# Kernel optimization log

Hardware: AMD Instinct MI355X
Metric: run time of the kernel (lower is better)

## Reference

```python
import jax, jax.numpy as jnp
import numpy as np

B, S, D = 4, 2048, 1024
H = 16
HD = D // H

def setup_inputs() -> dict:
    key = jax.random.key(0)
    ks = jax.random.split(key, 6)
    scale = 0.02
    return {
        "x": jax.random.normal(ks[0], (B, S, D), dtype=jnp.float32),
        "W_q": jax.random.normal(ks[1], (D, D), dtype=jnp.float32) * scale,
        "W_k": jax.random.normal(ks[2], (D, D), dtype=jnp.float32) * scale,
        "W_v": jax.random.normal(ks[3], (D, D), dtype=jnp.float32) * scale,
        "W_o": jax.random.normal(ks[4], (D, D), dtype=jnp.float32) * scale,
        "b_o": jax.random.normal(ks[5], (D,), dtype=jnp.float32) * scale,
    }

def reference(x, W_q, W_k, W_v, W_o, b_o):
    b, s, d = x.shape
    # projections, split heads: [b, h, s, hd]
    q = (x @ W_q).reshape(b, s, H, HD).transpose(0, 2, 1, 3)
    k = (x @ W_k).reshape(b, s, H, HD).transpose(0, 2, 1, 3)
    v = (x @ W_v).reshape(b, s, H, HD).transpose(0, 2, 1, 3)
    scores = jnp.einsum('bhqd,bhkd->bhqk', q, k)
    causal = jnp.triu(jnp.ones((s, s), dtype=bool), k=1)
    scores = jnp.where(causal, -jnp.inf, scores)
    # module divides by sqrt(hd) after masking; -inf stays -inf
    attn = jax.nn.softmax(scores / jnp.sqrt(jnp.float32(HD)), axis=-1)
    ctx = jnp.einsum('bhqk,bhkd->bhqd', attn, v)
    ctx = ctx.transpose(0, 2, 1, 3).reshape(b, s, d)
    return ctx @ W_o + b_o
```

## Files before the change

### kernel.cpp

```cpp
#include <hip/hip_runtime.h>
#include <hip/hip_bf16.h>
#include <math.h>

typedef __attribute__((ext_vector_type(8))) short bf16x8;
typedef __attribute__((ext_vector_type(4))) float f32x4;
typedef unsigned short u16;
typedef __hip_bfloat16 HB;

#define B_ 4
#define S_ 2048
#define D_ 1024
#define H_ 16
#define HD_ 64

__device__ __forceinline__ u16 f2b(float f) {
  HB h = __float2bfloat16(f);
  return *reinterpret_cast<u16*>(&h);
}
__device__ __forceinline__ void store1(HB* p, float v) { *p = __float2bfloat16(v); }
__device__ __forceinline__ void store1(float* p, float v) { *p = v; }

__device__ __forceinline__ float fexp2(float x) {
#if __has_builtin(__builtin_amdgcn_exp2f)
  return __builtin_amdgcn_exp2f(x);
#else
  return exp2f(x);
#endif
}

__device__ __forceinline__ void glds16(const u16* g, u16* l) {
  __builtin_amdgcn_global_load_lds(
      (const __attribute__((address_space(1))) void*)g,
      (__attribute__((address_space(3))) void*)l, 16, 0, 0);
}

__global__ __launch_bounds__(256) void cast_x(const float* __restrict__ xin,
                                              u16* __restrict__ xout) {
  const long i0 = ((long)blockIdx.x * 256 + threadIdx.x) * 8;
  bf16x8 r;
#pragma unroll
  for (int j = 0; j < 8; ++j) r[j] = (short)f2b(xin[i0 + j]);
  *(bf16x8*)(xout + i0) = r;
}

__global__ __launch_bounds__(256) void transpose_w(
    const float* __restrict__ w0, const float* __restrict__ w1,
    const float* __restrict__ w2, const float* __restrict__ w3,
    u16* __restrict__ out) {
  __shared__ __align__(16) u16 T[64 * 72];
  const float* Ws[4] = {w0, w1, w2, w3};
  const float* W = Ws[blockIdx.z];
  u16* Wt = out + (long)blockIdx.z * (1 << 20);
  const int t = threadIdx.x;
  const int r = t >> 3;
  const int c8 = (t & 7) * 8;
#pragma unroll
  for (int it = 0; it < 2; ++it) {
    const int row = blockIdx.y * 64 + it * 32 + r;
    const float* src = W + (long)row * D_ + blockIdx.x * 64 + c8;
#pragma unroll
    for (int j = 0; j < 8; ++j) T[(c8 + j) * 72 + it * 32 + r] = f2b(src[j]);
  }
  __syncthreads();
#pragma unroll
  for (int it = 0; it < 2; ++it) {
    const int row = it * 32 + r;
    bf16x8 v = *(const bf16x8*)(&T[row * 72 + c8]);
    *(bf16x8*)(Wt + (long)(blockIdx.x * 64 + row) * D_ + blockIdx.y * 64 + c8) = v;
  }
}

template <typename OT>
__global__ __launch_bounds__(256) void gemm_bt128d(
    const u16* __restrict__ A, const u16* __restrict__ BTb, long bt_stride,
    OT* __restrict__ Cb, long c_stride, const float* __restrict__ bias,
    u16* __restrict__ vt, int scale_q, int M, int N, int K) {
  const int flat = ((int)blockIdx.z << 9) + ((int)blockIdx.y << 3) + blockIdx.x;
  const int cpx = ((int)gridDim.z << 9) >> 3;
  const int nf = (flat & 7) * cpx + (flat >> 3);
  const int bz = nf >> 9;
  const int rem = nf & 511;
  const int by = rem >> 3, bx = rem & 7;

  const u16* BT = BTb + (long)bz * bt_stride;
  OT* C = Cb + (long)bz * c_stride;

  __shared__ __align__(16) u16 As[2][128 * 64];
  __shared__ __align__(16) u16 Bs[2][128 * 64];

  const int tid = threadIdx.x;
  const int w = tid >> 6, lane = tid & 63;
  const int qr = lane & 15, quad = lane >> 4;
  const int wm = w >> 1, wn = w & 1;

  const long rowA0 = (long)by * 128;
  const long rowB0 = (long)bx * 128;

  const int sr8 = lane >> 3;
  const int sc8 = ((lane & 7) ^ sr8) * 8;

  f32x4 acc[4][4] = {};

#define STAGE(nb, k0)                                                      \
  {                                                                        \
    _Pragma("unroll") for (int t = 0; t < 4; ++t) {                        \
      const int r = w * 32 + t * 8;                                        \
      glds16(A + (rowA0 + r + sr8) * K + (k0) + sc8, &As[nb][r * 64]);     \
      glds16(BT + (rowB0 + r + sr8) * K + (k0) + sc8, &Bs[nb][r * 64]);    \
    }                                                                      \
  }

  STAGE(0, 0);
  __syncthreads();

  const int NT = K >> 6;
  for (int kt = 0; kt < NT; ++kt) {
    const int b = kt & 1;
    if (kt + 1 < NT) STAGE(b ^ 1, (kt + 1) << 6);

#pragma unroll
    for (int kk = 0; kk < 2; ++kk) {
      bf16x8 af[4], bf[4];
#pragma unroll
      for (int ms = 0; ms < 4; ++ms) {
        const int m = wm * 64 + ms * 16 + qr;
        af[ms] = *(const bf16x8*)(&As[b][m * 64 +
                                         (((kk * 4 + quad) ^ (m & 7)) * 8)]);
      }
#pragma unroll
      for (int ns = 0; ns < 4; ++ns) {
        const int n = wn * 64 + ns * 16 + qr;
        bf[ns] = *(const bf16x8*)(&Bs[b][n * 64 +
                                         (((kk * 4 + quad) ^ (n & 7)) * 8)]);
      }
#pragma unroll
      for (int ms = 0; ms < 4; ++ms)
#pragma unroll
        for (int ns = 0; ns < 4; ++ns)
          acc[ms][ns] = __builtin_amdgcn_mfma_f32_16x16x32_bf16(
              af[ms], bf[ns], acc[ms][ns], 0, 0, 0);
    }
    __syncthreads();
  }
#undef STAGE

  if (vt && bz == 2) {
#pragma unroll
    for (int ns = 0; ns < 4; ++ns) {
      const int col = (int)rowB0 + wn * 64 + ns * 16 + qr;
#pragma unroll
      for (int ms = 0; ms < 4; ++ms) {
        const long row = rowA0 + wm * 64 + ms * 16 + quad * 4;
        const long b = row >> 11, s = row & 2047;
        ushort4 pk;
        pk.x = f2b(acc[ms][ns][0]); pk.y = f2b(acc[ms][ns][1]);
        pk.z = f2b(acc[ms][ns][2]); pk.w = f2b(acc[ms][ns][3]);
        *(ushort4*)(vt + ((b * H_ + (col >> 6)) * HD_ + (col & 63)) * S_ + s) = pk;
      }
    }
    return;
  }

  const float qs = (scale_q && bz == 0) ? 0.18033688011112042f : 1.f;
#pragma unroll
  for (int ns = 0; ns < 4; ++ns) {
    const long col = rowB0 + wn * 64 + ns * 16 + qr;
    const float bv = bias ? bias[col] : 0.f;
#pragma unroll
    for (int ms = 0; ms < 4; ++ms) {
      const long row = rowA0 + wm * 64 + ms * 16 + quad * 4;
#pragma unroll
      for (int r = 0; r < 4; ++r)
        store1(&C[(row + r) * (long)N + col], acc[ms][ns][r] * qs + bv);
    }
  }
}

__global__ __launch_bounds__(256) void attn12(
    const u16* __restrict__ Q, const u16* __restrict__ Kg,
    const u16* __restrict__ Vt, u16* __restrict__ ctx) {
  __shared__ __align__(16) u16 KV[2][2][64 * 64];
  __shared__ __align__(16) u16 Pl[4][16 * 64];

  const int tid = threadIdx.x;
  const int w = tid >> 6, lane = tid & 63;
  const int qr = lane & 15, quad = lane >> 4;
  const int bh = blockIdx.x;
  const int b = bh >> 4, h = bh & 15;

  const long baseQK = ((long)b * S_) * D_ + h * HD_;
  const long baseVt = (long)bh * HD_ * S_;

  const int sr8 = lane >> 3;
  const int sc8 = ((lane & 7) ^ sr8) * 8;

  bf16x8 vones;
#pragma unroll
  for (int j = 0; j < 8; ++j) vones[j] = (short)0x3F80;

  const int tiles2[2] = {(int)blockIdx.y, 15 - (int)blockIdx.y};

#pragma unroll
  for (int ti = 0; ti < 2; ++ti) {
    const int q0 = tiles2[ti] * 128;
    const int qbase = q0 + w * 32;

    bf16x8 aq[2][2];
#pragma unroll
    for (int i = 0; i < 2; ++i) {
      const u16* qp_ = Q + baseQK + (long)(qbase + i * 16 + qr) * D_;
      aq[i][0] = *(const bf16x8*)(qp_ + quad * 8);
      aq[i][1] = *(const bf16x8*)(qp_ + 32 + quad * 8);
    }

    f32x4 li[2] = {};
    f32x4 o[2][4] = {};

    const int nkt = q0 / 64 + 2;

#pragma unroll
    for (int t = 0; t < 2; ++t) {
      const int r = t * 32 + w * 8 + sr8;
      glds16(Kg + baseQK + (long)r * D_ + sc8, &KV[0][0][(t * 32 + w * 8) * 64]);
      glds16(Vt + baseVt + (long)r * S_ + sc8, &KV[0][1][(t * 32 + w * 8) * 64]);
    }

    for (int kt = 0; kt < nkt; ++kt) {
      const int kbase = kt * 64;
      const int buf = kt & 1;

      __syncthreads();

      if (kt + 1 < nkt) {
        const int nb = kbase + 64;
#pragma unroll
        for (int t = 0; t < 2; ++t) {
          const int r = t * 32 + w * 8 + sr8;
          glds16(Kg + baseQK + (long)(nb + r) * D_ + sc8,
                 &KV[buf ^ 1][0][(t * 32 + w * 8) * 64]);
          glds16(Vt + baseVt + (long)r * S_ + nb + sc8,
                 &KV[buf ^ 1][1][(t * 32 + w * 8) * 64]);
        }
      }

      const u16* Ksb = KV[buf][0];
      const u16* Vsb = KV[buf][1];

      bf16x8 kf[4][2];
#pragma unroll
      for (int ns = 0; ns < 4; ++ns) {
        const int row = ns * 16 + qr;
        kf[ns][0] = *(const bf16x8*)(&Ksb[row * 64 + ((quad ^ (row & 7)) * 8)]);
        kf[ns][1] =
            *(const bf16x8*)(&Ksb[row * 64 + (((4 + quad) ^ (row & 7)) * 8)]);
      }

      f32x4 s[2][4] = {};
#pragma unroll
      for (int i = 0; i < 2; ++i)
#pragma unroll
        for (int ns = 0; ns < 4; ++ns) {
          s[i][ns] = __builtin_amdgcn_mfma_f32_16x16x32_bf16(
              kf[ns][0], aq[i][0], s[i][ns], 0, 0, 0);
          s[i][ns] = __builtin_amdgcn_mfma_f32_16x16x32_bf16(
              kf[ns][1], aq[i][1], s[i][ns], 0, 0, 0);
        }

#pragma unroll
      for (int i = 0; i < 2; ++i) {
        if (kbase + 64 > qbase + i * 16) {
          const int qrow = qbase + i * 16 + qr;
#pragma unroll
          for (int ns = 0; ns < 4; ++ns) {
            const int kc = kbase + ns * 16 + quad * 4;
#pragma unroll
            for (int r = 0; r < 4; ++r)
              if (kc + r > qrow) s[i][ns][r] = -1.0e30f;
          }
        }
      }

      bf16x8 vf[4][2];
#pragma unroll
      for (int ns = 0; ns < 4; ++ns) {
        const int row = ns * 16 + qr;
        vf[ns][0] = *(const bf16x8*)(&Vsb[row * 64 + ((quad ^ (row & 7)) * 8)]);
        vf[ns][1] =
            *(const bf16x8*)(&Vsb[row * 64 + (((4 + quad) ^ (row & 7)) * 8)]);
      }

#pragma unroll
      for (int i = 0; i < 2; ++i) {
#pragma unroll
        for (int ns = 0; ns < 4; ++ns) {
          ushort4 pk;
          pk.x = f2b(fexp2(s[i][ns][0]));
          pk.y = f2b(fexp2(s[i][ns][1]));
          pk.z = f2b(fexp2(s[i][ns][2]));
          pk.w = f2b(fexp2(s[i][ns][3]));
          *(ushort4*)(&Pl[w][qr * 64 +
                             (((2 * ns + (quad >> 1)) ^ (qr & 7)) * 8) +
                             (quad & 1) * 4]) = pk;
        }

        bf16x8 pf0 = *(const bf16x8*)(&Pl[w][qr * 64 + ((quad ^ (qr & 7)) * 8)]);
        bf16x8 pf1 =
            *(const bf16x8*)(&Pl[w][qr * 64 + (((4 + quad) ^ (qr & 7)) * 8)]);
#pragma unroll
        for (int ns = 0; ns < 4; ++ns) {
          o[i][ns] = __builtin_amdgcn_mfma_f32_16x16x32_bf16(pf0, vf[ns][0],
                                                             o[i][ns], 0, 0, 0);
          o[i][ns] = __builtin_amdgcn_mfma_f32_16x16x32_bf16(pf1, vf[ns][1],
                                                             o[i][ns], 0, 0, 0);
        }
        li[i] =
            __builtin_amdgcn_mfma_f32_16x16x32_bf16(pf0, vones, li[i], 0, 0, 0);
        li[i] =
            __builtin_amdgcn_mfma_f32_16x16x32_bf16(pf1, vones, li[i], 0, 0, 0);
      }
    }

#pragma unroll
    for (int i = 0; i < 2; ++i)
#pragma unroll
      for (int r = 0; r < 4; ++r) {
        const float inv = 1.f / li[i][r];
        const long row = qbase + i * 16 + quad * 4 + r;
#pragma unroll
        for (int ns = 0; ns < 4; ++ns)
          ctx[((long)b * S_ + row) * D_ + h * HD_ + ns * 16 + qr] =
              f2b(o[i][ns][r] * inv);
      }
  }
}

extern "C" void kernel_launch(void* const* d_in, const int* in_sizes, int n_in,
                              void* d_out, int out_size, void* d_ws,
                              size_t ws_size, hipStream_t stream) {
  const float* x  = (const float*)d_in[0];
  const float* Wq = (const float*)d_in[1];
  const float* Wk = (const float*)d_in[2];
  const float* Wv = (const float*)d_in[3];
  const float* Wo = (const float*)d_in[4];
  const float* bo = (const float*)d_in[5];

  u16* ws = (u16*)d_ws;
  u16* xb  = ws;
  u16* Wt  = xb + 8388608l;
  u16* Qb  = Wt + 4l * 1048576;
  u16* Kb  = Qb + 8388608l;
  u16* Vb  = Kb + 8388608l;
  u16* ctx = Qb;

  cast_x<<<4096, 256, 0, stream>>>(x, xb);

  transpose_w<<<dim3(16, 16, 4), 256, 0, stream>>>(Wq, Wk, Wv, Wo, Wt);

  gemm_bt128d<HB><<<dim3(8, 64, 3), 256, 0, stream>>>(
      xb, Wt, 1048576l, (HB*)Qb, 8388608l, nullptr, Vb, 1, 8192, 1024, 1024);

  attn12<<<dim3(64, 8), 256, 0, stream>>>(Qb, Kb, Vb, ctx);

  gemm_bt128d<float><<<dim3(8, 64, 1), 256, 0, stream>>>(
      ctx, Wt + 3l * 1048576, 0, (float*)d_out, 0, bo, nullptr, 0,
      8192, 1024, 1024);
}
```

Measured before the change: 246.6 us.

## Use triple-buffered K=32 GEMM pipeline with vmcnt waits and one barrier

Restructures the projection and output GEMMs from a double-buffered K=64 loop to a three-stage K=32 ring of LDS buffers. Global-to-LDS loads run two tiles ahead, and each iteration waits with an explicit s_waitcnt vmcnt plus a single barrier instead of two __syncthreads. The aim is to hide load latency better, cut LDS use (which may allow higher occupancy) and remove a barrier per tile. In exchange there are twice as many iterations, each doing half the MFMA work per barrier, and the swizzle changes for the 32-wide rows.

Measured after the change: 261.9 us. 6.2% more time.

```diff
diff --git a/kernel.cpp b/kernel.cpp
--- a/kernel.cpp
+++ b/kernel.cpp
@@ -71,7 +71,7 @@
 }
 
 template <typename OT>
-__global__ __launch_bounds__(256) void gemm_bt128d(
+__global__ __launch_bounds__(256) void gemm_bt128p(
     const u16* __restrict__ A, const u16* __restrict__ BTb, long bt_stride,
     OT* __restrict__ Cb, long c_stride, const float* __restrict__ bias,
     u16* __restrict__ vt, int scale_q, int M, int N, int K) {
@@ -85,8 +85,8 @@
   const u16* BT = BTb + (long)bz * bt_stride;
   OT* C = Cb + (long)bz * c_stride;
 
-  __shared__ __align__(16) u16 As[2][128 * 64];
-  __shared__ __align__(16) u16 Bs[2][128 * 64];
+  __shared__ __align__(16) u16 As[3][128 * 32];
+  __shared__ __align__(16) u16 Bs[3][128 * 32];
 
   const int tid = threadIdx.x;
   const int w = tid >> 6, lane = tid & 63;
@@ -96,51 +96,61 @@
   const long rowA0 = (long)by * 128;
   const long rowB0 = (long)bx * 128;
 
-  const int sr8 = lane >> 3;
-  const int sc8 = ((lane & 7) ^ sr8) * 8;
+  const int sr = lane >> 2;
+  const int sc8 = ((lane & 3) ^ ((lane >> 3) & 3)) * 8;
+  const long arow = rowA0 + w * 16 + sr;
+  const long brow = rowB0 + w * 16 + sr;
 
   f32x4 acc[4][4] = {};
 
-#define STAGE(nb, k0)                                                      \
-  {                                                                        \
-    _Pragma("unroll") for (int t = 0; t < 4; ++t) {                        \
-      const int r = w * 32 + t * 8;                                        \
-      glds16(A + (rowA0 + r + sr8) * K + (k0) + sc8, &As[nb][r * 64]);     \
-      glds16(BT + (rowB0 + r + sr8) * K + (k0) + sc8, &Bs[nb][r * 64]);    \
-    }                                                                      \
+#define STAGE(nb, k0)                                                        \
+  {                                                                          \
+    glds16(A + arow * K + (k0) + sc8, &As[nb][(w * 16) * 32]);               \
+    glds16(A + (arow + 64) * K + (k0) + sc8, &As[nb][(64 + w * 16) * 32]);   \
+    glds16(BT + brow * K + (k0) + sc8, &Bs[nb][(w * 16) * 32]);              \
+    glds16(BT + (brow + 64) * K + (k0) + sc8, &Bs[nb][(64 + w * 16) * 32]);  \
   }
 
   STAGE(0, 0);
-  __syncthreads();
-
-  const int NT = K >> 6;
+  STAGE(1, 32);
+
+  const int NT = K >> 5;
+  int cur = 0;
   for (int kt = 0; kt < NT; ++kt) {
-    const int b = kt & 1;
-    if (kt + 1 < NT) STAGE(b ^ 1, (kt + 1) << 6);
-
-#pragma unroll
-    for (int kk = 0; kk < 2; ++kk) {
-      bf16x8 af[4], bf[4];
-#pragma unroll
-      for (int ms = 0; ms < 4; ++ms) {
-        const int m = wm * 64 + ms * 16 + qr;
-        af[ms] = *(const bf16x8*)(&As[b][m * 64 +
-                                         (((kk * 4 + quad) ^ (m & 7)) * 8)]);
-      }
-#pragma unroll
-      for (int ns = 0; ns < 4; ++ns) {
-        const int n = wn * 64 + ns * 16 + qr;
-        bf[ns] = *(const bf16x8*)(&Bs[b][n * 64 +
-                                         (((kk * 4 + quad) ^ (n & 7)) * 8)]);
-      }
-#pragma unroll
-      for (int ms = 0; ms < 4; ++ms)
-#pragma unroll
-        for (int ns = 0; ns < 4; ++ns)
-          acc[ms][ns] = __builtin_amdgcn_mfma_f32_16x16x32_bf16(
-              af[ms], bf[ns], acc[ms][ns], 0, 0, 0);
-    }
-    __syncthreads();
+    if (kt + 1 < NT) {
+      asm volatile("s_waitcnt vmcnt(4)" ::: "memory");
+    } else {
+      asm volatile("s_waitcnt vmcnt(0)" ::: "memory");
+    }
+    __builtin_amdgcn_s_barrier();
+    __builtin_amdgcn_sched_barrier(0);
+
+    if (kt + 2 < NT) {
+      int nb = cur + 2;
+      if (nb >= 3) nb -= 3;
+      STAGE(nb, (kt + 2) << 5);
+    }
+
+    bf16x8 af[4], bf[4];
+#pragma unroll
+    for (int ms = 0; ms < 4; ++ms) {
+      const int m = wm * 64 + ms * 16 + qr;
+      af[ms] = *(const bf16x8*)(&As[cur][m * 32 + ((quad ^ ((m >> 1) & 3)) * 8)]);
+    }
+#pragma unroll
+    for (int ns = 0; ns < 4; ++ns) {
+      const int n = wn * 64 + ns * 16 + qr;
+      bf[ns] = *(const bf16x8*)(&Bs[cur][n * 32 + ((quad ^ ((n >> 1) & 3)) * 8)]);
+    }
+
+#pragma unroll
+    for (int ms = 0; ms < 4; ++ms)
+#pragma unroll
+      for (int ns = 0; ns < 4; ++ns)
+        acc[ms][ns] = __builtin_amdgcn_mfma_f32_16x16x32_bf16(
+            af[ms], bf[ns], acc[ms][ns], 0, 0, 0);
+
+    cur = (cur + 1 == 3) ? 0 : cur + 1;
   }
 #undef STAGE
 
@@ -356,12 +366,12 @@
 
   transpose_w<<<dim3(16, 16, 4), 256, 0, stream>>>(Wq, Wk, Wv, Wo, Wt);
 
-  gemm_bt128d<HB><<<dim3(8, 64, 3), 256, 0, stream>>>(
+  gemm_bt128p<HB><<<dim3(8, 64, 3), 256, 0, stream>>>(
       xb, Wt, 1048576l, (HB*)Qb, 8388608l, nullptr, Vb, 1, 8192, 1024, 1024);
 
   attn12<<<dim3(64, 8), 256, 0, stream>>>(Qb, Kb, Vb, ctx);
 
-  gemm_bt128d<float><<<dim3(8, 64, 1), 256, 0, stream>>>(
+  gemm_bt128p<float><<<dim3(8, 64, 1), 256, 0, stream>>>(
       ctx, Wt + 3l * 1048576, 0, (float*)d_out, 0, bo, nullptr, 0,
       8192, 1024, 1024);
 }
```
